# Optimization experiments

Measured on AMD Instinct MI355X. Metric: run time of the kernel, lower is better.

## Reference

```python
import jax, jax.numpy as jnp
import numpy as np

N, IN_DIM, OUT_DIM = 8192, 512, 256

def setup_inputs() -> dict:
    key = jax.random.key(0)
    k1, k2, k3, k4, k5 = jax.random.split(key, 5)
    feat = jax.random.normal(k1, (N, IN_DIM), dtype=jnp.float32)
    counting_attn = jax.random.uniform(k2, (N, N), dtype=jnp.float32)
    Wq = jax.random.normal(k3, (IN_DIM, OUT_DIM), dtype=jnp.float32) * (IN_DIM ** -0.5)
    Wk = jax.random.normal(k4, (IN_DIM, OUT_DIM), dtype=jnp.float32) * (IN_DIM ** -0.5)
    Wv = jax.random.normal(k5, (IN_DIM, OUT_DIM), dtype=jnp.float32) * (IN_DIM ** -0.5)
    return {"feat": feat, "counting_attn": counting_attn, "Wq": Wq, "Wk": Wk, "Wv": Wv}

def reference(feat, counting_attn, Wq, Wk, Wv):
    # eval mode: feat_drop / attn_drop are identity
    Q = feat @ Wq  # [N, D]
    K = feat @ Wk
    V = feat @ Wv
    scale = 1.0 / jnp.sqrt(jnp.float32(Q.shape[1]))
    logits = (Q @ K.T) * scale  # [N, N]
    logits = logits - jnp.max(logits, axis=1, keepdims=True)
    a_nomi = jnp.exp(logits) * counting_attn
    a_deno = jnp.sum(a_nomi, axis=1, keepdims=True)
    a_nor = a_nomi / (a_deno + 1e-9)
    ret = a_nor @ V  # [N, D]
    return jax.nn.elu(ret)
```

## Files before the change

kernel.cpp:

```cpp
#include <hip/hip_runtime.h>

typedef unsigned short u16;
typedef unsigned int u32;
typedef __attribute__((ext_vector_type(8))) __bf16 bf16x8;
typedef __attribute__((ext_vector_type(16))) float f32x16;

#define NN 8192
#define IND 512
#define DD 256
#define LN_K 0.00195122595f

__device__ __forceinline__ void gl_lds16(const void* g, void* l) {
  __builtin_amdgcn_global_load_lds((const __attribute__((address_space(1))) void*)g,
                                   (__attribute__((address_space(3))) void*)l, 16, 0, 0);
}
__device__ __forceinline__ u16 bf16_rne(float x) {
  u32 u = __float_as_uint(x);
  u += 0x7FFF + ((u >> 16) & 1);
  return (u16)(u >> 16);
}

__global__ __launch_bounds__(256) void wt_transpose(const float* __restrict__ Wq,
                                                    const float* __restrict__ Wk,
                                                    const float* __restrict__ Wv,
                                                    u16* __restrict__ WT) {
  const int o = blockIdx.y;
  const int e = blockIdx.x * 256 + threadIdx.x;
  const int n = e >> 9, k = e & 511;
  const float* W = (o == 0) ? Wq : ((o == 1) ? Wk : Wv);
  WT[o * (DD * IND) + e] = bf16_rne(W[k * DD + n]);
}

__global__ __launch_bounds__(256) void cvt_feat(const float* __restrict__ f,
                                                u16* __restrict__ fb) {
  const int i = (blockIdx.x * 256 + threadIdx.x) * 4;
  float4 v = *(const float4*)(f + i);
  u32 lo = (u32)bf16_rne(v.x) | ((u32)bf16_rne(v.y) << 16);
  u32 hi = (u32)bf16_rne(v.z) | ((u32)bf16_rne(v.w) << 16);
  *(uint2*)(fb + i) = make_uint2(lo, hi);
}

__global__ __launch_bounds__(256, 2) void proj_qkv(const u16* __restrict__ featb,
                                                   const u16* __restrict__ WT,
                                                   u16* __restrict__ Qs,
                                                   u16* __restrict__ Ks,
                                                   u16* __restrict__ VTs) {
  __shared__ u16 tl[4][32 * 40];
  const int mb = blockIdx.x, o = blockIdx.y;
  const int wave = threadIdx.x >> 6, lane = threadIdx.x & 63;
  const int mm = lane & 31, h = lane >> 5;
  const int m0 = mb * 128 + wave * 32;
  const u16* wt = WT + o * (DD * IND);

  f32x16 acc[8];
#pragma unroll
  for (int nt = 0; nt < 8; ++nt)
#pragma unroll
    for (int r = 0; r < 16; ++r) acc[nt][r] = 0.f;

  for (int kc = 0; kc < 32; ++kc) {
    bf16x8 af = *(const bf16x8*)(featb + (size_t)(m0 + mm) * IND + kc * 16 + 8 * h);
#pragma unroll
    for (int nt = 0; nt < 8; ++nt) {
      bf16x8 bf = *(const bf16x8*)(wt + (size_t)(nt * 32 + mm) * IND + kc * 16 + 8 * h);
      acc[nt] = __builtin_amdgcn_mfma_f32_32x32x16_bf16(af, bf, acc[nt], 0, 0, 0);
    }
  }

  if (o < 2) {
    const float sc = (o == 0) ? 0.0625f : 1.f;
    u16* dst = (o == 0) ? Qs : Ks;
#pragma unroll
    for (int nt = 0; nt < 8; ++nt)
#pragma unroll
      for (int r = 0; r < 16; ++r) {
        const int mrow = (r & 3) + 8 * (r >> 2) + 4 * h;
        dst[(size_t)(m0 + mrow) * DD + nt * 32 + mm] = bf16_rne(acc[nt][r] * sc);
      }
  } else {
    const int n2 = lane >> 1, mh = lane & 1;
    for (int nt = 0; nt < 8; ++nt) {
#pragma unroll
      for (int r = 0; r < 16; r += 2) {
        const int mrow = (r & 3) + 8 * (r >> 2) + 4 * h;
        u32 pk = (u32)bf16_rne(acc[nt][r]) | ((u32)bf16_rne(acc[nt][r + 1]) << 16);
        *(u32*)(&tl[wave][mm * 40 + mrow]) = pk;
      }
      __syncthreads();
      bf16x8 t0 = *(const bf16x8*)(&tl[wave][n2 * 40 + mh * 16]);
      bf16x8 t1 = *(const bf16x8*)(&tl[wave][n2 * 40 + mh * 16 + 8]);
      u16* gp = VTs + (size_t)(nt * 32 + n2) * NN + m0 + mh * 16;
      *(bf16x8*)(gp) = t0;
      *(bf16x8*)(gp + 8) = t1;
      __syncthreads();
    }
  }
}

__global__ __launch_bounds__(256, 2) void flash_attn(const u16* __restrict__ Qs,
                                                     const u16* __restrict__ Ks,
                                                     const u16* __restrict__ VTs,
                                                     const float* __restrict__ cnt,
                                                     float* __restrict__ ml,
                                                     float* __restrict__ Op,
                                                     int jiters) {
  __shared__ u16 kl[2][8192];
  __shared__ u16 vl[2][8192];
  const int rb = blockIdx.x, sp = blockIdx.y;
  const int wave = threadIdx.x >> 6, lane = threadIdx.x & 63;
  const int mm = lane & 31, h = lane >> 5;
  const int m0 = rb * 128 + wave * 32;
  const int jbase = sp * jiters * 32;

  const int Lw = lane;

  bf16x8 qf[16];
  {
    const u16* qrow = Qs + (size_t)(m0 + mm) * DD;
#pragma unroll
    for (int c = 0; c < 16; ++c) qf[c] = *(const bf16x8*)(qrow + c * 16 + 8 * h);
  }
  f32x16 acc[8];
#pragma unroll
  for (int nt = 0; nt < 8; ++nt)
#pragma unroll
    for (int r = 0; r < 16; ++r) acc[nt][r] = 0.f;
  float m_run = -1e30f, l_run = 0.f;

#pragma unroll
  for (int ii = 0; ii < 4; ++ii) {
    const int w = wave * 4 + ii;
    const int L = w * 64 + Lw;
    gl_lds16(Ks + (size_t)(jbase + (L & 31)) * DD + (L >> 5) * 8, (char*)kl + w * 1024);
    gl_lds16(VTs + (size_t)(L & 255) * NN + jbase + (L >> 8) * 8, (char*)vl + w * 1024);
  }
  __syncthreads();

  for (int jb = 0; jb < jiters; ++jb) {
    const int buf = jb & 1;
    const int j0 = jbase + jb * 32;
    if (jb + 1 < jiters) {
      const int jn = j0 + 32;
#pragma unroll
      for (int ii = 0; ii < 4; ++ii) {
        const int w = wave * 4 + ii;
        const int L = w * 64 + Lw;
        gl_lds16(Ks + (size_t)(jn + (L & 31)) * DD + (L >> 5) * 8,
                 (char*)kl + (buf ^ 1) * 16384 + w * 1024);
        gl_lds16(VTs + (size_t)(L & 255) * NN + jn + (L >> 8) * 8,
                 (char*)vl + (buf ^ 1) * 16384 + w * 1024);
      }
    }
    float cf[16];
    {
      const float* crow = cnt + (size_t)(m0 + mm) * NN + j0 + 4 * h;
#pragma unroll
      for (int g = 0; g < 4; ++g) {
        float4 t = *(const float4*)(crow + 8 * g);
        cf[4 * g + 0] = t.x;
        cf[4 * g + 1] = t.y;
        cf[4 * g + 2] = t.z;
        cf[4 * g + 3] = t.w;
      }
    }

    const char* klb = (const char*)kl + buf * 16384;
    const char* vlb = (const char*)vl + buf * 16384;
    f32x16 sv0, sv1;
#pragma unroll
    for (int r = 0; r < 16; ++r) { sv0[r] = 0.f; sv1[r] = 0.f; }
#pragma unroll
    for (int c = 0; c < 16; c += 2) {
      bf16x8 kf0 = *(const bf16x8*)(klb + (((2 * c + h) * 32 + mm) << 4));
      bf16x8 kf1 = *(const bf16x8*)(klb + (((2 * c + 2 + h) * 32 + mm) << 4));
      sv0 = __builtin_amdgcn_mfma_f32_32x32x16_bf16(kf0, qf[c], sv0, 0, 0, 0);
      sv1 = __builtin_amdgcn_mfma_f32_32x32x16_bf16(kf1, qf[c + 1], sv1, 0, 0, 0);
    }
    f32x16 sv = sv0 + sv1;

    float mx = sv[0];
#pragma unroll
    for (int r = 1; r < 16; ++r) mx = fmaxf(mx, sv[r]);
    mx = fmaxf(mx, __shfl_xor(mx, 32));
    const float m_new = fmaxf(m_run, mx);
    const bool upd = __any(mx > m_run);
    const float msub = m_new - LN_K;

    float p[16];
    float bsum = 0.f;
#pragma unroll
    for (int r = 0; r < 16; ++r) {
      p[r] = __expf(sv[r] - msub) * cf[r];
      bsum += p[r];
    }
    bsum += __shfl_xor(bsum, 32);

    if (upd) {
      const float alpha = __expf(m_run - m_new);
      l_run = l_run * alpha + bsum;
#pragma unroll
      for (int nt = 0; nt < 8; ++nt)
#pragma unroll
        for (int r = 0; r < 16; ++r) acc[nt][r] *= alpha;
    } else {
      l_run += bsum;
    }
    m_run = m_new;

    u32 P2[8];
#pragma unroll
    for (int j = 0; j < 8; ++j) {
      const u32 ua = __float_as_uint(p[2 * j]);
      const u32 ub = __float_as_uint(p[2 * j + 1]);
      P2[j] = (ua >> 16) | (ub & 0xFFFF0000u);
    }
#pragma unroll
    for (int kc2 = 0; kc2 < 2; ++kc2) {
      union { u32 u[4]; bf16x8 v; } pf;
#pragma unroll
      for (int tp = 0; tp < 4; ++tp) {
        const int src = mm + 32 * (tp >> 1);
        const u32 va = __shfl(P2[4 * kc2 + (tp & 1)], src);
        const u32 vb = __shfl(P2[4 * kc2 + 2 + (tp & 1)], src);
        pf.u[tp] = h ? vb : va;
      }
#pragma unroll
      for (int nt = 0; nt < 8; ++nt) {
        bf16x8 vf = *(const bf16x8*)(vlb + ((((2 * kc2 + h) * 256) + nt * 32 + mm) << 4));
        acc[nt] = __builtin_amdgcn_mfma_f32_32x32x16_bf16(vf, pf.v, acc[nt], 0, 0, 0);
      }
    }
    __syncthreads();
  }

  const int wb = rb * 4 + wave;
  if (lane < 32) {
    ml[((sp * 256 + wb) << 6) + lane] = m_run;
    ml[((sp * 256 + wb) << 6) + 32 + lane] = l_run;
  }
#pragma unroll
  for (int nt = 0; nt < 8; ++nt) {
#pragma unroll
    for (int rr = 0; rr < 4; ++rr) {
      float* op = Op + ((((size_t)(sp * 256 + wb) * 8 + nt) * 4 + rr) * 64 + lane) * 4;
      float4 v = make_float4(acc[nt][4 * rr], acc[nt][4 * rr + 1],
                             acc[nt][4 * rr + 2], acc[nt][4 * rr + 3]);
      *(float4*)op = v;
    }
  }
}

__global__ __launch_bounds__(256) void merge_out(const float* __restrict__ ml,
                                                 const float* __restrict__ Op,
                                                 float* __restrict__ out,
                                                 int spl) {
  const int wid = blockIdx.x * 4 + (threadIdx.x >> 6);
  const int lane = threadIdx.x & 63, mm = lane & 31, h = lane >> 5;
  const int wb = wid >> 3, nt = wid & 7;
  float mv[8], lv[8], wsc[8];
  for (int s = 0; s < spl; ++s) {
    mv[s] = ml[((s * 256 + wb) << 6) + mm];
    lv[s] = ml[((s * 256 + wb) << 6) + 32 + mm];
  }
  float M = mv[0];
  for (int s = 1; s < spl; ++s) M = fmaxf(M, mv[s]);
  float L = 0.f;
  for (int s = 0; s < spl; ++s) {
    wsc[s] = __expf(mv[s] - M);
    L += wsc[s] * lv[s];
  }
  const float inv = 1.f / (L + 1e-9f);

  float o[16];
#pragma unroll
  for (int r = 0; r < 16; ++r) o[r] = 0.f;
  for (int s = 0; s < spl; ++s) {
#pragma unroll
    for (int rr = 0; rr < 4; ++rr) {
      const float* op = Op + ((((size_t)(s * 256 + wb) * 8 + nt) * 4 + rr) * 64 + lane) * 4;
      float4 v = *(const float4*)op;
      o[4 * rr + 0] += wsc[s] * v.x;
      o[4 * rr + 1] += wsc[s] * v.y;
      o[4 * rr + 2] += wsc[s] * v.z;
      o[4 * rr + 3] += wsc[s] * v.w;
    }
  }
  const int row = wb * 32 + mm;
#pragma unroll
  for (int g = 0; g < 4; ++g) {
    float4 v;
    float* pv = &v.x;
#pragma unroll
    for (int i = 0; i < 4; ++i) {
      float t = o[4 * g + i] * inv;
      pv[i] = t > 0.f ? t : expm1f(t);
    }
    *(float4*)(out + (size_t)row * DD + nt * 32 + 8 * g + 4 * h) = v;
  }
}

extern "C" void kernel_launch(void* const* d_in, const int* in_sizes, int n_in,
                              void* d_out, int out_size, void* d_ws, size_t ws_size,
                              hipStream_t stream) {
  const float* feat = (const float*)d_in[0];
  const float* cnta = (const float*)d_in[1];
  const float* Wq = (const float*)d_in[2];
  const float* Wk = (const float*)d_in[3];
  const float* Wv = (const float*)d_in[4];
  char* ws = (char*)d_ws;
  u16* WT = (u16*)(ws);
  u16* featb = (u16*)(ws + (1ull << 20));
  u16* Qs = (u16*)(ws + (9ull << 20));
  u16* Ks = (u16*)(ws + (13ull << 20));
  u16* VTs = (u16*)(ws + (17ull << 20));
  float* ml = (float*)(ws + (21ull << 20));
  float* Op = (float*)(ws + (22ull << 20));
  float* out = (float*)d_out;

  const size_t need8 = (22ull << 20) + (64ull << 20);
  const int spl = (ws_size >= need8) ? 8 : 4;
  const int jiters = NN / (spl * 32);

  hipLaunchKernelGGL(wt_transpose, dim3(512, 3), dim3(256), 0, stream, Wq, Wk, Wv, WT);
  hipLaunchKernelGGL(cvt_feat, dim3(4096), dim3(256), 0, stream, feat, featb);
  hipLaunchKernelGGL(proj_qkv, dim3(64, 3), dim3(256), 0, stream, featb, WT, Qs, Ks, VTs);
  hipLaunchKernelGGL(flash_attn, dim3(64, spl), dim3(256), 0, stream, Qs, Ks, VTs, cnta, ml, Op,
                     jiters);
  hipLaunchKernelGGL(merge_out, dim3(512), dim3(256), 0, stream, ml, Op, out, spl);
}
```

Measured before the change: 577.0 us.

## Stage counting_attn tiles through LDS via async loads, add MFMA priority and split-major grid

The counting_attn tile is now prefetched for the next iteration with asynchronous global-to-LDS loads into a swizzled shared buffer. Previously each lane read it directly from global memory right before use, which stalled on latency. MFMA sections are wrapped in s_setprio to favour matrix issue. The grid is flattened so consecutive blocks share a row block across splits, which may improve cache locality. The added 16KB of LDS may reduce occupancy, and the single-buffered cl relies on an lgkmcnt wait to avoid a read-after-write hazard.

```diff
diff --git a/kernel.cpp b/kernel.cpp
--- a/kernel.cpp
+++ b/kernel.cpp
@@ -103,16 +103,21 @@
                                                      const float* __restrict__ cnt,
                                                      float* __restrict__ ml,
                                                      float* __restrict__ Op,
-                                                     int jiters) {
+                                                     int jiters, int spl) {
   __shared__ u16 kl[2][8192];
   __shared__ u16 vl[2][8192];
-  const int rb = blockIdx.x, sp = blockIdx.y;
+  __shared__ float cl[4096];
+  const int bid = blockIdx.x;
+  const int lg = __ffs(spl) - 1;
+  const int sp = bid & (spl - 1);
+  const int rb = bid >> lg;
   const int wave = threadIdx.x >> 6, lane = threadIdx.x & 63;
   const int mm = lane & 31, h = lane >> 5;
   const int m0 = rb * 128 + wave * 32;
   const int jbase = sp * jiters * 32;
 
-  const int Lw = lane;
+  const int crow = lane >> 3;
+  const int ccol = 4 * ((lane & 7) ^ (lane >> 3));
 
   bf16x8 qf[16];
   {
@@ -130,37 +135,48 @@
 #pragma unroll
   for (int ii = 0; ii < 4; ++ii) {
     const int w = wave * 4 + ii;
-    const int L = w * 64 + Lw;
+    const int L = w * 64 + lane;
     gl_lds16(Ks + (size_t)(jbase + (L & 31)) * DD + (L >> 5) * 8, (char*)kl + w * 1024);
     gl_lds16(VTs + (size_t)(L & 255) * NN + jbase + (L >> 8) * 8, (char*)vl + w * 1024);
+    gl_lds16(cnt + (size_t)(rb * 128 + w * 8 + crow) * NN + jbase + ccol,
+             (char*)cl + w * 1024);
   }
   __syncthreads();
 
   for (int jb = 0; jb < jiters; ++jb) {
     const int buf = jb & 1;
     const int j0 = jbase + jb * 32;
+
+    float cf[16];
+    {
+      const char* cr = (const char*)cl + (wave * 32 + mm) * 128;
+#pragma unroll
+      for (int g = 0; g < 4; ++g) {
+        float4 t = *(const float4*)(cr + (((16 * h + 32 * g) ^ ((mm & 7) << 4))));
+        cf[4 * g + 0] = t.x;
+        cf[4 * g + 1] = t.y;
+        cf[4 * g + 2] = t.z;
+        cf[4 * g + 3] = t.w;
+      }
+    }
+
     if (jb + 1 < jiters) {
       const int jn = j0 + 32;
 #pragma unroll
       for (int ii = 0; ii < 4; ++ii) {
         const int w = wave * 4 + ii;
-        const int L = w * 64 + Lw;
+        const int L = w * 64 + lane;
         gl_lds16(Ks + (size_t)(jn + (L & 31)) * DD + (L >> 5) * 8,
                  (char*)kl + (buf ^ 1) * 16384 + w * 1024);
         gl_lds16(VTs + (size_t)(L & 255) * NN + jn + (L >> 8) * 8,
                  (char*)vl + (buf ^ 1) * 16384 + w * 1024);
       }
-    }
-    float cf[16];
-    {
-      const float* crow = cnt + (size_t)(m0 + mm) * NN + j0 + 4 * h;
-#pragma unroll
-      for (int g = 0; g < 4; ++g) {
-        float4 t = *(const float4*)(crow + 8 * g);
-        cf[4 * g + 0] = t.x;
-        cf[4 * g + 1] = t.y;
-        cf[4 * g + 2] = t.z;
-        cf[4 * g + 3] = t.w;
+      asm volatile("s_waitcnt lgkmcnt(0)" ::: "memory");
+#pragma unroll
+      for (int ii = 0; ii < 4; ++ii) {
+        const int w = wave * 4 + ii;
+        gl_lds16(cnt + (size_t)(rb * 128 + w * 8 + crow) * NN + jn + ccol,
+                 (char*)cl + w * 1024);
       }
     }
 
@@ -169,6 +185,7 @@
     f32x16 sv0, sv1;
 #pragma unroll
     for (int r = 0; r < 16; ++r) { sv0[r] = 0.f; sv1[r] = 0.f; }
+    __builtin_amdgcn_s_setprio(1);
 #pragma unroll
     for (int c = 0; c < 16; c += 2) {
       bf16x8 kf0 = *(const bf16x8*)(klb + (((2 * c + h) * 32 + mm) << 4));
@@ -176,6 +193,7 @@
       sv0 = __builtin_amdgcn_mfma_f32_32x32x16_bf16(kf0, qf[c], sv0, 0, 0, 0);
       sv1 = __builtin_amdgcn_mfma_f32_32x32x16_bf16(kf1, qf[c + 1], sv1, 0, 0, 0);
     }
+    __builtin_amdgcn_s_setprio(0);
     f32x16 sv = sv0 + sv1;
 
     float mx = sv[0];
@@ -224,11 +242,13 @@
         const u32 vb = __shfl(P2[4 * kc2 + 2 + (tp & 1)], src);
         pf.u[tp] = h ? vb : va;
       }
+      __builtin_amdgcn_s_setprio(1);
 #pragma unroll
       for (int nt = 0; nt < 8; ++nt) {
         bf16x8 vf = *(const bf16x8*)(vlb + ((((2 * kc2 + h) * 256) + nt * 32 + mm) << 4));
         acc[nt] = __builtin_amdgcn_mfma_f32_32x32x16_bf16(vf, pf.v, acc[nt], 0, 0, 0);
       }
+      __builtin_amdgcn_s_setprio(0);
     }
     __syncthreads();
   }
@@ -324,7 +344,7 @@
   hipLaunchKernelGGL(wt_transpose, dim3(512, 3), dim3(256), 0, stream, Wq, Wk, Wv, WT);
   hipLaunchKernelGGL(cvt_feat, dim3(4096), dim3(256), 0, stream, feat, featb);
   hipLaunchKernelGGL(proj_qkv, dim3(64, 3), dim3(256), 0, stream, featb, WT, Qs, Ks, VTs);
-  hipLaunchKernelGGL(flash_attn, dim3(64, spl), dim3(256), 0, stream, Qs, Ks, VTs, cnta, ml, Op,
-                     jiters);
+  hipLaunchKernelGGL(flash_attn, dim3(64 * spl), dim3(256), 0, stream, Qs, Ks, VTs, cnta, ml,
+                     Op, jiters, spl);
   hipLaunchKernelGGL(merge_out, dim3(512), dim3(256), 0, stream, ml, Op, out, spl);
 }
```

New measurement: 651.2 us. +12.9%, slower.
